# Performance work log

Measured on AMD Instinct MI355X. Metric: run time of the kernel, lower is better.

## Reference

```python
import jax, jax.numpy as jnp
import numpy as np

D_HEAD = 64
IGNORE = -100000.0


def setup_inputs() -> dict:
    key = jax.random.key(0)
    ks = jax.random.split(key, 5)
    B, S, D, H, M = 2, 2048, 768, 12, D_HEAD
    scale = 0.05  # 'random_normal' keras init stddev
    return {
        "x": jax.random.normal(ks[0], (B, S, D), jnp.float32),
        "W_Q": jax.random.normal(ks[1], (H, D, M), jnp.float32) * scale,
        "b_Q": jnp.zeros((H, M), jnp.float32),
        "W_K": jax.random.normal(ks[2], (H, D, M), jnp.float32) * scale,
        "b_K": jnp.zeros((H, M), jnp.float32),
        "W_V": jax.random.normal(ks[3], (H, D, M), jnp.float32) * scale,
        "b_V": jnp.zeros((H, M), jnp.float32),
        "W_O": jax.random.normal(ks[4], (H, M, D), jnp.float32) * scale,
        "b_O": jnp.zeros((D,), jnp.float32),
    }


def reference(x, W_Q, b_Q, W_K, b_K, W_V, b_V, W_O, b_O):
    # q,k,v: [b, s, h, m]
    q = jnp.einsum("bqd,hdm->bqhm", x, W_Q) + b_Q
    k = jnp.einsum("bkd,hdm->bkhm", x, W_K) + b_K
    v = jnp.einsum("bkd,hdm->bkhm", x, W_V) + b_V
    # scores: [b, h, q, k], scaled by 1/sqrt(d_head)
    scores = jnp.einsum("bqhm,bkhm->bhqk", q, k) / jnp.sqrt(
        jnp.asarray(D_HEAD, q.dtype)
    )
    S = x.shape[1]
    # causal mask: strictly-upper-triangular positions set to IGNORE (-1e5),
    # matching tf.where(mask == 1, IGNORE, scores)
    causal = jnp.arange(S)[:, None] >= jnp.arange(S)[None, :]  # [q, k]
    scores = jnp.where(causal[None, None, :, :], scores, jnp.asarray(IGNORE, scores.dtype))
    pattern = jax.nn.softmax(scores, axis=-1)
    z = jnp.einsum("bhqk,bkhm->bqhm", pattern, v)
    attn_out = jnp.einsum("bqhm,hmd->bqd", z, W_O) + b_O
    return attn_out
```

## Files before the change

kernel.cpp:

```cpp
#include <hip/hip_runtime.h>
#include <hip/hip_bf16.h>
#include <cstdint>
#include <cstddef>

#define B_ 2
#define S_ 2048
#define D_ 768
#define H_ 12
#define M_ 64
#define BS_ (B_ * S_)
#define NQKV_ 2304
#define NCHUNK_ 80
#define TOTCHUNK_ (24 * NCHUNK_)

typedef __attribute__((ext_vector_type(8))) short bf16x8;
typedef __attribute__((ext_vector_type(4))) float f32x4;

__device__ __forceinline__ unsigned short f2bu(float f) {
    __hip_bfloat16 h = __float2bfloat16(f);
    unsigned short u;
    __builtin_memcpy(&u, &h, 2);
    return u;
}
__device__ __forceinline__ unsigned pack2(float a, float b) {
    return (unsigned)f2bu(a) | ((unsigned)f2bu(b) << 16);
}

__device__ __forceinline__ bf16x8 ld16(const unsigned short* p) {
    p = (const unsigned short*)__builtin_assume_aligned(p, 16);
    bf16x8 v; __builtin_memcpy(&v, p, 16); return v;
}
__device__ __forceinline__ uint4 ld16u(const unsigned short* p) {
    p = (const unsigned short*)__builtin_assume_aligned(p, 16);
    uint4 v; __builtin_memcpy(&v, p, 16); return v;
}
__device__ __forceinline__ void st16(unsigned short* p, uint4 v) {
    p = (unsigned short*)__builtin_assume_aligned(p, 16);
    __builtin_memcpy(p, &v, 16);
}
__device__ __forceinline__ void st8(unsigned short* p, uint2 v) {
    p = (unsigned short*)__builtin_assume_aligned(p, 8);
    __builtin_memcpy(p, &v, 8);
}
__device__ __forceinline__ float4 ldf4(const float* p) {
    p = (const float*)__builtin_assume_aligned(p, 16);
    float4 v; __builtin_memcpy(&v, p, 16); return v;
}
__device__ __forceinline__ void async16(const unsigned short* g, unsigned short* l) {
    __builtin_amdgcn_global_load_lds(
        (const __attribute__((address_space(1))) void*)g,
        (__attribute__((address_space(3))) void*)l, 16, 0, 0);
}
__device__ __forceinline__ void b82f(uint4 u, float* o) {
    o[0] = __uint_as_float(u.x << 16); o[1] = __uint_as_float(u.x & 0xffff0000u);
    o[2] = __uint_as_float(u.y << 16); o[3] = __uint_as_float(u.y & 0xffff0000u);
    o[4] = __uint_as_float(u.z << 16); o[5] = __uint_as_float(u.z & 0xffff0000u);
    o[6] = __uint_as_float(u.w << 16); o[7] = __uint_as_float(u.w & 0xffff0000u);
}

#define NEG_BIG (-3.0e38f)

__global__ void prep(const float* __restrict__ WQ, const float* __restrict__ WK,
                     const float* __restrict__ WV, const float* __restrict__ WO,
                     const float* __restrict__ x,
                     unsigned short* __restrict__ WT,
                     unsigned short* __restrict__ WOT,
                     unsigned short* __restrict__ xb)
{
    const int bx = blockIdx.x;
    if (bx < 216) {
        const int xx = bx % 9, yy = bx / 9;
        const int c  = xx * 256 + threadIdx.x;
        const int k0 = yy * 32;
        const int which = c / D_;
        const int r = c - which * D_;
        const int h = r >> 6, m = r & 63;
        const float* Wsel = (which == 0) ? WQ : (which == 1) ? WK : WV;
        const float* src = Wsel + (size_t)h * D_ * M_ + m;
        unsigned short* dst = WT + (size_t)c * D_ + k0;
        for (int i = 0; i < 32; i += 8) {
            float wv[8];
#pragma unroll
            for (int j = 0; j < 8; j++) wv[j] = src[(size_t)(k0 + i + j) * M_];
            uint4 pu;
            pu.x = pack2(wv[0], wv[1]); pu.y = pack2(wv[2], wv[3]);
            pu.z = pack2(wv[4], wv[5]); pu.w = pack2(wv[6], wv[7]);
            st16(dst + i, pu);
        }
    } else if (bx < 288) {
        const int b2 = bx - 216;
        const int xx = b2 % 3, yy = b2 / 3;
        const int c  = xx * 256 + threadIdx.x;
        const int k0 = yy * 32;
        unsigned short* dst = WOT + (size_t)c * D_ + k0;
        for (int i = 0; i < 32; i += 8) {
            float wv[8];
#pragma unroll
            for (int j = 0; j < 8; j++) wv[j] = WO[(size_t)(k0 + i + j) * D_ + c];
            uint4 pu;
            pu.x = pack2(wv[0], wv[1]); pu.y = pack2(wv[2], wv[3]);
            pu.z = pack2(wv[4], wv[5]); pu.w = pack2(wv[6], wv[7]);
            st16(dst + i, pu);
        }
    } else {
        const size_t i = ((size_t)(bx - 288) * 256 + threadIdx.x) * 16;
#pragma unroll
        for (int p = 0; p < 2; p++) {
            float4 a0 = ldf4(x + i + p * 8), a1 = ldf4(x + i + p * 8 + 4);
            uint4 u;
            u.x = pack2(a0.x, a0.y); u.y = pack2(a0.z, a0.w);
            u.z = pack2(a1.x, a1.y); u.w = pack2(a1.z, a1.w);
            st16(xb + i + p * 8, u);
        }
    }
}

__global__ __launch_bounds__(256, 2) void qkv_gemm(
    const unsigned short* __restrict__ xb,
    const unsigned short* __restrict__ WT,
    const float* __restrict__ bQ, const float* __restrict__ bK,
    const float* __restrict__ bV,
    unsigned short* __restrict__ qo, unsigned short* __restrict__ ko,
    unsigned short* __restrict__ vt)
{
    const int row0 = blockIdx.x * 128;
    const int col0 = blockIdx.y * 128;
    const int t = threadIdx.x;
    const int w = t >> 6, lane = t & 63, quad = lane >> 4, l16 = lane & 15;
    const int wrow0 = (w & 1) * 64, wcol0 = (w >> 1) * 64;

    __shared__ unsigned short Alds[128 * 64];
    __shared__ unsigned short Blds[128 * 64];

    f32x4 acc[4][4] = {};

    const unsigned short* asrc[4];
    const unsigned short* bsrc[4];
    int ldsoff[4];
#pragma unroll
    for (int q = 0; q < 4; q++) {
        const int cq = w * 256 + q * 64 + lane;
        const int row = cq >> 3, c = cq & 7;
        const int cs = c ^ (row & 7);
        asrc[q] = xb + (size_t)(row0 + row) * D_ + cs * 8;
        bsrc[q] = WT + (size_t)(col0 + row) * D_ + cs * 8;
        ldsoff[q] = (w * 256 + q * 64) * 8;
    }
    const int swz = (l16 & 7);

    for (int k0 = 0; k0 < D_; k0 += 64) {
#pragma unroll
        for (int q = 0; q < 4; q++) async16(asrc[q] + k0, Alds + ldsoff[q]);
#pragma unroll
        for (int q = 0; q < 4; q++) async16(bsrc[q] + k0, Blds + ldsoff[q]);
        __syncthreads();

        bf16x8 af[4][2], bfm[4][2];
#pragma unroll
        for (int rt = 0; rt < 4; rt++) {
            const int row = wrow0 + rt * 16 + l16;
#pragma unroll
            for (int hh = 0; hh < 2; hh++)
                af[rt][hh] = ld16(&Alds[row * 64 + ((hh * 4 + quad) ^ swz) * 8]);
        }
#pragma unroll
        for (int st = 0; st < 4; st++) {
            const int row = wcol0 + st * 16 + l16;
#pragma unroll
            for (int hh = 0; hh < 2; hh++)
                bfm[st][hh] = ld16(&Blds[row * 64 + ((hh * 4 + quad) ^ swz) * 8]);
        }
#pragma unroll
        for (int rt = 0; rt < 4; rt++)
#pragma unroll
            for (int st = 0; st < 4; st++) {
                acc[rt][st] = __builtin_amdgcn_mfma_f32_16x16x32_bf16(
                    af[rt][0], bfm[st][0], acc[rt][st], 0, 0, 0);
                acc[rt][st] = __builtin_amdgcn_mfma_f32_16x16x32_bf16(
                    af[rt][1], bfm[st][1], acc[rt][st], 0, 0, 0);
            }
        __syncthreads();
    }

    const int which = col0 / D_;
    const int colin = col0 - which * D_;

    if (which < 2) {
        const float* bias = (which == 0) ? bQ : bK;
        unsigned short* outp = (which == 0) ? qo : ko;
        const float scale = (which == 0) ? 0.125f : 1.0f;
#pragma unroll
        for (int st = 0; st < 4; st++) {
            const int cl = colin + wcol0 + st * 16 + l16;
            const int h = cl >> 6, m = cl & 63;
            const float bval = bias[cl];
#pragma unroll
            for (int rt = 0; rt < 4; rt++)
#pragma unroll
                for (int rr = 0; rr < 4; rr++) {
                    const int R = row0 + wrow0 + rt * 16 + quad * 4 + rr;
                    const int bb = R >> 11, s = R & (S_ - 1);
                    outp[(((size_t)bb * H_ + h) * S_ + s) * M_ + m] =
                        f2bu((acc[rt][st][rr] + bval) * scale);
                }
        }
    } else {
#pragma unroll
        for (int st = 0; st < 4; st++) {
            const int cl = colin + wcol0 + st * 16 + l16;
            const int h = cl >> 6, m = cl & 63;
            const float bval = bV[cl];
#pragma unroll
            for (int rt = 0; rt < 4; rt++) {
                const int R0 = row0 + wrow0 + rt * 16 + quad * 4;
                const int bb = R0 >> 11, s0 = R0 & (S_ - 1);
                uint2 v;
                v.x = pack2(acc[rt][st][0] + bval, acc[rt][st][1] + bval);
                v.y = pack2(acc[rt][st][2] + bval, acc[rt][st][3] + bval);
                st8(&vt[(((size_t)bb * H_ + h) * M_ + m) * S_ + s0], v);
            }
        }
    }
}

struct StageRegs { uint4 ka[4]; uint4 va[4]; };

__device__ __forceinline__ void load_tile(const unsigned short* kb,
                                          const unsigned short* vb,
                                          int t, StageRegs& s)
{
#pragma unroll
    for (int q = 0; q < 4; q++) {
        const int ci = q * 256 + t;
        s.ka[q] = ld16u(kb + (size_t)(ci >> 3) * M_ + (ci & 7) * 8);
    }
#pragma unroll
    for (int q = 0; q < 4; q++) {
        const int ci = q * 256 + t;
        s.va[q] = ld16u(vb + (size_t)(ci >> 4) * S_ + (ci & 15) * 8);
    }
}

__global__ __launch_bounds__(256, 3) void attn_split(
    const unsigned short* __restrict__ Q,
    const unsigned short* __restrict__ Kin,
    const unsigned short* __restrict__ Vt,
    unsigned short* __restrict__ Opart,
    float* __restrict__ ml)
{
    const int xx = blockIdx.x;
    const int bh = blockIdx.y;

    int qt, c, nc;
    if (xx < 8)       { qt = xx; c = 0; nc = 1; }
    else if (xx < 24) { int u = xx - 8;  qt = 8  + (u >> 1); c = u & 1;  nc = 2; }
    else if (xx < 48) { int u = xx - 24; qt = 16 + u / 3;    c = u % 3;  nc = 3; }
    else              { int u = xx - 48; qt = 24 + (u >> 2); c = u & 3;  nc = 4; }

    const int ci     = bh * NCHUNK_ + xx;
    const int kbeg   = c * 512;
    const int keyend = min((qt + 1) * 64, kbeg + 512);
    const int iters  = (keyend - kbeg + 127) >> 7;
    const bool lastchunk = (c == nc - 1);

    const int t = threadIdx.x;
    const int wave = t >> 6, lane = t & 63, quad = lane >> 4, l16 = lane & 15;

    const unsigned short* Qb  = Q   + ((size_t)bh * S_ + qt * 64) * M_;
    const unsigned short* Kb  = Kin + (size_t)bh * S_ * M_;
    const unsigned short* VtB = Vt  + (size_t)bh * M_ * S_;

    __shared__ unsigned short Klds[128][72];
    __shared__ unsigned short Vlds[64][136];
    __shared__ unsigned short Plds[4][16][132];

    bf16x8 qf[2];
    {
        const unsigned short* qrow = Qb + (size_t)(wave * 16 + l16) * M_;
        qf[0] = ld16(qrow + quad * 8);
        qf[1] = ld16(qrow + 32 + quad * 8);
    }

    f32x4 o_acc[4] = {};
    float mrow[4] = {NEG_BIG, NEG_BIG, NEG_BIG, NEG_BIG};
    float lrow[4] = {0.f, 0.f, 0.f, 0.f};

    StageRegs sr;
    load_tile(Kb + (size_t)kbeg * M_, VtB + kbeg, t, sr);

    for (int it = 0; it < iters; it++) {
        __syncthreads();
#pragma unroll
        for (int q = 0; q < 4; q++) {
            const int cq = q * 256 + t;
            st16(&Klds[cq >> 3][(cq & 7) * 8], sr.ka[q]);
        }
#pragma unroll
        for (int q = 0; q < 4; q++) {
            const int cq = q * 256 + t;
            st16(&Vlds[cq >> 4][(cq & 15) * 8], sr.va[q]);
        }
        __syncthreads();

        if (it + 1 < iters) {
            const int key1 = kbeg + (it + 1) * 128;
            load_tile(Kb + (size_t)key1 * M_, VtB + key1, t, sr);
        }

        f32x4 s_acc[8];
#pragma unroll
        for (int st = 0; st < 8; st++) {
            f32x4 z4 = {0.f, 0.f, 0.f, 0.f};
            bf16x8 kb0 = ld16(&Klds[st * 16 + l16][quad * 8]);
            bf16x8 kb1 = ld16(&Klds[st * 16 + l16][32 + quad * 8]);
            z4 = __builtin_amdgcn_mfma_f32_16x16x32_bf16(qf[0], kb0, z4, 0, 0, 0);
            z4 = __builtin_amdgcn_mfma_f32_16x16x32_bf16(qf[1], kb1, z4, 0, 0, 0);
            s_acc[st] = z4;
        }

        if (lastchunk && it == iters - 1) {
            const int key0 = kbeg + it * 128;
            const int qrow = qt * 64 + wave * 16 + quad * 4;
#pragma unroll
            for (int st = 0; st < 8; st++)
#pragma unroll
                for (int r = 0; r < 4; r++)
                    if (key0 + st * 16 + l16 > qrow + r)
                        s_acc[st][r] = -1e30f;
        }

        float rmax[4];
#pragma unroll
        for (int r = 0; r < 4; r++) {
            float m0 = fmaxf(fmaxf(s_acc[0][r], s_acc[1][r]),
                             fmaxf(s_acc[2][r], s_acc[3][r]));
            float m1 = fmaxf(fmaxf(s_acc[4][r], s_acc[5][r]),
                             fmaxf(s_acc[6][r], s_acc[7][r]));
            rmax[r] = fmaxf(m0, m1);
        }
#pragma unroll
        for (int off = 1; off < 16; off <<= 1)
#pragma unroll
            for (int r = 0; r < 4; r++)
                rmax[r] = fmaxf(rmax[r], __shfl_xor(rmax[r], off, 64));

        float mnew[4], alpha[4];
#pragma unroll
        for (int r = 0; r < 4; r++) {
            mnew[r]  = fmaxf(mrow[r], rmax[r]);
            alpha[r] = __expf(mrow[r] - mnew[r]);
            mrow[r]  = mnew[r];
        }

        float psum[4] = {0.f, 0.f, 0.f, 0.f};
#pragma unroll
        for (int st = 0; st < 8; st++) {
#pragma unroll
            for (int r = 0; r < 4; r++) {
                float p = __expf(s_acc[st][r] - mnew[r]);
                psum[r] += p;
                Plds[wave][quad * 4 + r][st * 16 + l16] = f2bu(p);
            }
        }
#pragma unroll
        for (int off = 1; off < 16; off <<= 1)
#pragma unroll
            for (int r = 0; r < 4; r++)
                psum[r] += __shfl_xor(psum[r], off, 64);

#pragma unroll
        for (int r = 0; r < 4; r++) lrow[r] = lrow[r] * alpha[r] + psum[r];
#pragma unroll
        for (int st = 0; st < 4; st++)
#pragma unroll
            for (int r = 0; r < 4; r++) o_acc[st][r] *= alpha[r];

        __syncthreads();

        bf16x8 pf[4];
#pragma unroll
        for (int cc = 0; cc < 4; cc++)
            pf[cc] = ld16(&Plds[wave][l16][cc * 32 + quad * 8]);
#pragma unroll
        for (int st = 0; st < 4; st++) {
#pragma unroll
            for (int cc = 0; cc < 4; cc++) {
                bf16x8 vb = ld16(&Vlds[st * 16 + l16][cc * 32 + quad * 8]);
                o_acc[st] = __builtin_amdgcn_mfma_f32_16x16x32_bf16(
                    pf[cc], vb, o_acc[st], 0, 0, 0);
            }
        }
    }

    unsigned short* Op = Opart + (size_t)ci * 4096;
#pragma unroll
    for (int st = 0; st < 4; st++)
#pragma unroll
        for (int r = 0; r < 4; r++) {
            const int q = wave * 16 + quad * 4 + r;
            Op[q * 64 + st * 16 + l16] = f2bu(o_acc[st][r]);
        }
    if (l16 == 0) {
#pragma unroll
        for (int r = 0; r < 4; r++) {
            const int q = wave * 16 + quad * 4 + r;
            ml[(size_t)ci * 128 + q]      = mrow[r];
            ml[(size_t)ci * 128 + 64 + q] = lrow[r];
        }
    }
}

__global__ void combine(const unsigned short* __restrict__ Opart,
                        const float* __restrict__ ml,
                        unsigned short* __restrict__ Z)
{
    const int qt = blockIdx.x, bh = blockIdx.y;
    const int b = bh / H_, h = bh - b * H_;
    const int g = qt >> 3, r7 = qt & 7;
    const int nc = g + 1;
    const int base = bh * NCHUNK_ + qt + 4 * g * (g - 1) + r7 * g;

    const int t = threadIdx.x;
    const int q = t >> 2, fs = (t & 3) * 16;

    float m_c[4], l_c[4];
    float M = NEG_BIG;
    for (int c = 0; c < nc; c++) {
        m_c[c] = ml[(size_t)(base + c) * 128 + q];
        l_c[c] = ml[(size_t)(base + c) * 128 + 64 + q];
        M = fmaxf(M, m_c[c]);
    }
    float L = 0.f;
    float w_c[4];
    for (int c = 0; c < nc; c++) {
        w_c[c] = __expf(m_c[c] - M);
        L += l_c[c] * w_c[c];
    }
    const float invL = 1.0f / L;

    float o[16] = {};
    for (int c = 0; c < nc; c++) {
        const unsigned short* op =
            Opart + (size_t)(base + c) * 4096 + q * 64 + fs;
        const float wc = w_c[c];
        float f[8];
        b82f(ld16u(op), f);
#pragma unroll
        for (int j = 0; j < 8; j++) o[j] += wc * f[j];
        b82f(ld16u(op + 8), f);
#pragma unroll
        for (int j = 0; j < 8; j++) o[8 + j] += wc * f[j];
    }

    unsigned short* zp =
        Z + ((size_t)b * S_ + qt * 64 + q) * (H_ * M_) + h * M_ + fs;
    uint4 u0, u1;
    u0.x = pack2(o[0]*invL,  o[1]*invL);  u0.y = pack2(o[2]*invL,  o[3]*invL);
    u0.z = pack2(o[4]*invL,  o[5]*invL);  u0.w = pack2(o[6]*invL,  o[7]*invL);
    u1.x = pack2(o[8]*invL,  o[9]*invL);  u1.y = pack2(o[10]*invL, o[11]*invL);
    u1.z = pack2(o[12]*invL, o[13]*invL); u1.w = pack2(o[14]*invL, o[15]*invL);
    st16(zp, u0);
    st16(zp + 8, u1);
}

__global__ __launch_bounds__(256, 2) void oproj_gemm(
    const unsigned short* __restrict__ Zin,
    const unsigned short* __restrict__ WOT,
    const float* __restrict__ bO,
    float* __restrict__ out)
{
    const int row0 = blockIdx.x * 128;
    const int col0 = blockIdx.y * 128;
    const int t = threadIdx.x;
    const int w = t >> 6, lane = t & 63, quad = lane >> 4, l16 = lane & 15;
    const int wrow0 = (w & 1) * 64, wcol0 = (w >> 1) * 64;

    __shared__ unsigned short Alds[128 * 64];
    __shared__ unsigned short Blds[128 * 64];

    f32x4 acc[4][4] = {};

    const unsigned short* asrc[4];
    const unsigned short* bsrc[4];
    int ldsoff[4];
#pragma unroll
    for (int q = 0; q < 4; q++) {
        const int cq = w * 256 + q * 64 + lane;
        const int row = cq >> 3, c = cq & 7;
        const int cs = c ^ (row & 7);
        asrc[q] = Zin + (size_t)(row0 + row) * D_ + cs * 8;
        bsrc[q] = WOT + (size_t)(col0 + row) * D_ + cs * 8;
        ldsoff[q] = (w * 256 + q * 64) * 8;
    }
    const int swz = (l16 & 7);

    for (int k0 = 0; k0 < D_; k0 += 64) {
#pragma unroll
        for (int q = 0; q < 4; q++) async16(asrc[q] + k0, Alds + ldsoff[q]);
#pragma unroll
        for (int q = 0; q < 4; q++) async16(bsrc[q] + k0, Blds + ldsoff[q]);
        __syncthreads();

        bf16x8 af[4][2], bfm[4][2];
#pragma unroll
        for (int rt = 0; rt < 4; rt++) {
            const int row = wrow0 + rt * 16 + l16;
#pragma unroll
            for (int hh = 0; hh < 2; hh++)
                af[rt][hh] = ld16(&Alds[row * 64 + ((hh * 4 + quad) ^ swz) * 8]);
        }
#pragma unroll
        for (int st = 0; st < 4; st++) {
            const int row = wcol0 + st * 16 + l16;
#pragma unroll
            for (int hh = 0; hh < 2; hh++)
                bfm[st][hh] = ld16(&Blds[row * 64 + ((hh * 4 + quad) ^ swz) * 8]);
        }
#pragma unroll
        for (int rt = 0; rt < 4; rt++)
#pragma unroll
            for (int st = 0; st < 4; st++) {
                acc[rt][st] = __builtin_amdgcn_mfma_f32_16x16x32_bf16(
                    af[rt][0], bfm[st][0], acc[rt][st], 0, 0, 0);
                acc[rt][st] = __builtin_amdgcn_mfma_f32_16x16x32_bf16(
                    af[rt][1], bfm[st][1], acc[rt][st], 0, 0, 0);
            }
        __syncthreads();
    }

#pragma unroll
    for (int st = 0; st < 4; st++) {
        const int c = col0 + wcol0 + st * 16 + l16;
        const float bval = bO[c];
#pragma unroll
        for (int rt = 0; rt < 4; rt++)
#pragma unroll
            for (int rr = 0; rr < 4; rr++) {
                const int R = row0 + wrow0 + rt * 16 + quad * 4 + rr;
                out[(size_t)R * D_ + c] = acc[rt][st][rr] + bval;
            }
    }
}

extern "C" void kernel_launch(void* const* d_in, const int* in_sizes, int n_in,
                              void* d_out, int out_size, void* d_ws, size_t ws_size,
                              hipStream_t stream)
{
    const float* x  = (const float*)d_in[0];
    const float* WQ = (const float*)d_in[1];
    const float* bQ = (const float*)d_in[2];
    const float* WK = (const float*)d_in[3];
    const float* bK = (const float*)d_in[4];
    const float* WV = (const float*)d_in[5];
    const float* bV = (const float*)d_in[6];
    const float* WO = (const float*)d_in[7];
    const float* bO = (const float*)d_in[8];
    float* out = (float*)d_out;

    const size_t n = (size_t)B_ * H_ * S_ * M_;
    unsigned short* q_ws  = (unsigned short*)d_ws;
    unsigned short* k_ws  = q_ws + n;
    unsigned short* vt_ws = k_ws + n;
    unsigned short* z_ws  = vt_ws + n;
    unsigned short* WT    = z_ws + n;
    unsigned short* WOT   = WT + (size_t)NQKV_ * D_;
    unsigned short* xb    = WOT + (size_t)D_ * D_;
    unsigned short* Opart = xb + (size_t)BS_ * D_;
    float* mlbuf = (float*)(Opart + (size_t)TOTCHUNK_ * 4096);

    prep<<<dim3(1056), 256, 0, stream>>>(WQ, WK, WV, WO, x, WT, WOT, xb);
    qkv_gemm<<<dim3(BS_ / 128, NQKV_ / 128), 256, 0, stream>>>(
        xb, WT, bQ, bK, bV, q_ws, k_ws, vt_ws);
    attn_split<<<dim3(NCHUNK_, B_ * H_), 256, 0, stream>>>(
        q_ws, k_ws, vt_ws, Opart, mlbuf);
    combine<<<dim3(S_ / 64, B_ * H_), 256, 0, stream>>>(Opart, mlbuf, z_ws);
    oproj_gemm<<<dim3(BS_ / 128, D_ / 128), 256, 0, stream>>>(
        z_ws, WOT, bO, out);
}
```

Baseline: 174.7 us.

## Transpose attention MFMA operands so each lane owns one query row

Swaps the A/B operands of the QK^T and PV MFMAs so the score and output accumulators are laid out with one query row per lane (l16) and keys along the 4-element register dimension. Row max and row sum then need only two cross-quad shuffles instead of four per row across 16 lanes, and the softmax state collapses to one scalar per lane. P tiles and output partials are written with packed 8-byte stores instead of scalar 2-byte stores, and the P LDS row pitch is changed from 132 to 136. This trims shuffle and LDS store instruction count in the inner loop, at the risk of different LDS bank-conflict behaviour on the new access pattern.

```diff
diff --git a/kernel.cpp b/kernel.cpp
--- a/kernel.cpp
+++ b/kernel.cpp
@@ -272,7 +272,7 @@
 
     __shared__ unsigned short Klds[128][72];
     __shared__ unsigned short Vlds[64][136];
-    __shared__ unsigned short Plds[4][16][132];
+    __shared__ unsigned short Plds[4][16][136];
 
     bf16x8 qf[2];
     {
@@ -282,8 +282,7 @@
     }
 
     f32x4 o_acc[4] = {};
-    float mrow[4] = {NEG_BIG, NEG_BIG, NEG_BIG, NEG_BIG};
-    float lrow[4] = {0.f, 0.f, 0.f, 0.f};
+    float mrow = NEG_BIG, lrow = 0.f;
 
     StageRegs sr;
     load_tile(Kb + (size_t)kbeg * M_, VtB + kbeg, t, sr);
@@ -313,100 +312,89 @@
             f32x4 z4 = {0.f, 0.f, 0.f, 0.f};
             bf16x8 kb0 = ld16(&Klds[st * 16 + l16][quad * 8]);
             bf16x8 kb1 = ld16(&Klds[st * 16 + l16][32 + quad * 8]);
-            z4 = __builtin_amdgcn_mfma_f32_16x16x32_bf16(qf[0], kb0, z4, 0, 0, 0);
-            z4 = __builtin_amdgcn_mfma_f32_16x16x32_bf16(qf[1], kb1, z4, 0, 0, 0);
+            z4 = __builtin_amdgcn_mfma_f32_16x16x32_bf16(kb0, qf[0], z4, 0, 0, 0);
+            z4 = __builtin_amdgcn_mfma_f32_16x16x32_bf16(kb1, qf[1], z4, 0, 0, 0);
             s_acc[st] = z4;
         }
 
         if (lastchunk && it == iters - 1) {
-            const int key0 = kbeg + it * 128;
-            const int qrow = qt * 64 + wave * 16 + quad * 4;
+            const int key0 = kbeg + it * 128 + quad * 4;
+            const int qg = qt * 64 + wave * 16 + l16;
 #pragma unroll
             for (int st = 0; st < 8; st++)
 #pragma unroll
                 for (int r = 0; r < 4; r++)
-                    if (key0 + st * 16 + l16 > qrow + r)
+                    if (key0 + st * 16 + r > qg)
                         s_acc[st][r] = -1e30f;
         }
 
-        float rmax[4];
-#pragma unroll
-        for (int r = 0; r < 4; r++) {
-            float m0 = fmaxf(fmaxf(s_acc[0][r], s_acc[1][r]),
-                             fmaxf(s_acc[2][r], s_acc[3][r]));
-            float m1 = fmaxf(fmaxf(s_acc[4][r], s_acc[5][r]),
-                             fmaxf(s_acc[6][r], s_acc[7][r]));
-            rmax[r] = fmaxf(m0, m1);
-        }
-#pragma unroll
-        for (int off = 1; off < 16; off <<= 1)
-#pragma unroll
-            for (int r = 0; r < 4; r++)
-                rmax[r] = fmaxf(rmax[r], __shfl_xor(rmax[r], off, 64));
-
-        float mnew[4], alpha[4];
-#pragma unroll
-        for (int r = 0; r < 4; r++) {
-            mnew[r]  = fmaxf(mrow[r], rmax[r]);
-            alpha[r] = __expf(mrow[r] - mnew[r]);
-            mrow[r]  = mnew[r];
-        }
-
-        float psum[4] = {0.f, 0.f, 0.f, 0.f};
+        float lmax = s_acc[0][0];
+#pragma unroll
+        for (int st = 0; st < 8; st++)
+#pragma unroll
+            for (int r = 0; r < 4; r++) lmax = fmaxf(lmax, s_acc[st][r]);
+        lmax = fmaxf(lmax, __shfl_xor(lmax, 16, 64));
+        lmax = fmaxf(lmax, __shfl_xor(lmax, 32, 64));
+
+        const float mnew = fmaxf(mrow, lmax);
+        const float alpha = __expf(mrow - mnew);
+        mrow = mnew;
+
+        float p[8][4];
+        float psum = 0.f;
+#pragma unroll
+        for (int st = 0; st < 8; st++)
+#pragma unroll
+            for (int r = 0; r < 4; r++) {
+                p[st][r] = __expf(s_acc[st][r] - mnew);
+                psum += p[st][r];
+            }
+        psum += __shfl_xor(psum, 16, 64);
+        psum += __shfl_xor(psum, 32, 64);
+        lrow = lrow * alpha + psum;
+
+#pragma unroll
+        for (int stf = 0; stf < 4; stf++)
+#pragma unroll
+            for (int r = 0; r < 4; r++) o_acc[stf][r] *= alpha;
+
 #pragma unroll
         for (int st = 0; st < 8; st++) {
-#pragma unroll
-            for (int r = 0; r < 4; r++) {
-                float p = __expf(s_acc[st][r] - mnew[r]);
-                psum[r] += p;
-                Plds[wave][quad * 4 + r][st * 16 + l16] = f2bu(p);
+            uint2 u;
+            u.x = pack2(p[st][0], p[st][1]);
+            u.y = pack2(p[st][2], p[st][3]);
+            st8(&Plds[wave][l16][st * 16 + quad * 4], u);
+        }
+
+        __syncthreads();
+
+        bf16x8 pt[4];
+#pragma unroll
+        for (int cc = 0; cc < 4; cc++)
+            pt[cc] = ld16(&Plds[wave][l16][cc * 32 + quad * 8]);
+#pragma unroll
+        for (int stf = 0; stf < 4; stf++) {
+#pragma unroll
+            for (int cc = 0; cc < 4; cc++) {
+                bf16x8 vb = ld16(&Vlds[stf * 16 + l16][cc * 32 + quad * 8]);
+                o_acc[stf] = __builtin_amdgcn_mfma_f32_16x16x32_bf16(
+                    vb, pt[cc], o_acc[stf], 0, 0, 0);
             }
         }
-#pragma unroll
-        for (int off = 1; off < 16; off <<= 1)
-#pragma unroll
-            for (int r = 0; r < 4; r++)
-                psum[r] += __shfl_xor(psum[r], off, 64);
-
-#pragma unroll
-        for (int r = 0; r < 4; r++) lrow[r] = lrow[r] * alpha[r] + psum[r];
-#pragma unroll
-        for (int st = 0; st < 4; st++)
-#pragma unroll
-            for (int r = 0; r < 4; r++) o_acc[st][r] *= alpha[r];
-
-        __syncthreads();
-
-        bf16x8 pf[4];
-#pragma unroll
-        for (int cc = 0; cc < 4; cc++)
-            pf[cc] = ld16(&Plds[wave][l16][cc * 32 + quad * 8]);
-#pragma unroll
-        for (int st = 0; st < 4; st++) {
-#pragma unroll
-            for (int cc = 0; cc < 4; cc++) {
-                bf16x8 vb = ld16(&Vlds[st * 16 + l16][cc * 32 + quad * 8]);
-                o_acc[st] = __builtin_amdgcn_mfma_f32_16x16x32_bf16(
-                    pf[cc], vb, o_acc[st], 0, 0, 0);
-            }
-        }
     }
 
     unsigned short* Op = Opart + (size_t)ci * 4096;
-#pragma unroll
-    for (int st = 0; st < 4; st++)
-#pragma unroll
-        for (int r = 0; r < 4; r++) {
-            const int q = wave * 16 + quad * 4 + r;
-            Op[q * 64 + st * 16 + l16] = f2bu(o_acc[st][r]);
-        }
-    if (l16 == 0) {
-#pragma unroll
-        for (int r = 0; r < 4; r++) {
-            const int q = wave * 16 + quad * 4 + r;
-            ml[(size_t)ci * 128 + q]      = mrow[r];
-            ml[(size_t)ci * 128 + 64 + q] = lrow[r];
-        }
+    const int q = wave * 16 + l16;
+#pragma unroll
+    for (int stf = 0; stf < 4; stf++) {
+        uint2 u;
+        u.x = pack2(o_acc[stf][0], o_acc[stf][1]);
+        u.y = pack2(o_acc[stf][2], o_acc[stf][3]);
+        st8(&Op[q * 64 + stf * 16 + quad * 4], u);
+    }
+    if (quad == 0) {
+        ml[(size_t)ci * 128 + q]      = mrow;
+        ml[(size_t)ci * 128 + 64 + q] = lrow;
     }
 }
 
```

After: 166.1 us. 1.05x faster.
